# Kernel optimization log

Hardware: AMD Instinct MI355X
Metric: run time of the kernel (lower is better)

Reference implementation:

```python
import jax, jax.numpy as jnp
import numpy as np

SEQ, N = 8192, 1024
W_SYN = 20.0

# ArcTan surrogate spike fn ('ArcTan', alpha=1.0, beta=10.0): forward = Heaviside
@jax.custom_vjp
def spike(x):
    return (x > 0).astype(x.dtype)

def _spike_fwd(x):
    return spike(x), x

def _spike_bwd(x, g):
    return (g * (1.0 / (1.0 + (10.0 * x) ** 2)),)

spike.defvjp(_spike_fwd, _spike_bwd)


def setup_inputs() -> dict:
    key = jax.random.key(0)
    k_in, = jax.random.split(key, 1)
    input_batch = jax.random.normal(k_in, (SEQ, N), dtype=jnp.float32)
    state = jnp.zeros((2, N), jnp.float32)  # (v, u)
    # learned params, sized per init_kwargs
    W1 = jnp.eye(N, dtype=jnp.float32) * W_SYN          # f1.ff.weight [N, N]
    W2 = jnp.ones((1, N), jnp.float32) * W_SYN          # f2.ff.weight [1, N]
    a = jnp.full((N,), 0.02, jnp.float32)
    b = jnp.full((N,), 0.2, jnp.float32)
    c = jnp.full((N,), -65.0, jnp.float32)
    d = jnp.full((N,), 8.0, jnp.float32)
    thresh = jnp.full((N,), 30.0, jnp.float32)
    dt = jnp.full((N,), 1.0, jnp.float32)               # time_step per neuron
    leak = jnp.full((1,), 0.99, jnp.float32)            # decode leak
    return dict(input_batch=input_batch, state=state, W1=W1, W2=W2,
                a=a, b=b, c=c, d=d, thresh=thresh, dt=dt, leak=leak)


def reference(input_batch, state, W1, W2, a, b, c, d, thresh, dt, leak):
    v0, u0 = state[0], state[1]
    dm0 = jnp.zeros((1,), input_batch.dtype)  # decode_mempot starts at 0

    def step(carry, x_t):
        v, u, dm = carry
        I = W1 @ x_t  # synaptic current [N]
        # Izhikevich ODE (Euler step)
        v_new = v + dt * (0.04 * v * v + 5.0 * v + 140.0 - u + I)
        u_new = u + dt * a * (b * v - u)
        s = spike(v_new - thresh)
        v_out = v_new * (1.0 - s) + c * s   # reset v -> c on spike
        u_out = u_new + d * s               # u -> u + d on spike
        dm_new = leak * dm + W2 @ s         # leaky-integrator decode [1]
        return (v_out, u_out, dm_new), (s, jnp.stack([v_out, u_out]), dm_new)

    _, (outputs, states, decoded) = jax.lax.scan(step, (v0, u0, dm0), input_batch)
    return outputs, states, decoded  # [T,N], [T,2,N], [T,1]
```

## Files before the change

kernel.cpp:

```cpp
#include <hip/hip_runtime.h>

#define CAP 32
#define K 32

__global__ void sparsify_kernel(const float* __restrict__ W1, int N,
                                int* __restrict__ cnts, int* __restrict__ cols,
                                float* __restrict__ wts) {
  __shared__ int scnt;
  const int row = blockIdx.x;
  if (threadIdx.x == 0) scnt = 0;
  __syncthreads();
  const float* wr = W1 + (long)row * N;
  for (int k = threadIdx.x; k < N; k += blockDim.x) {
    float w = wr[k];
    if (w != 0.0f) {
      int slot = atomicAdd(&scnt, 1);
      if (slot < CAP) {
        cols[row * CAP + slot] = k;
        wts[row * CAP + slot] = w;
      }
    }
  }
  __syncthreads();
  if (threadIdx.x == 0) {
    cnts[row] = scnt;
    if (scnt == 0) { cols[row * CAP] = 0; wts[row * CAP] = 0.0f; }
  }
}

__global__ void touch_kernel(const float4* __restrict__ x4, long n4,
                             float* __restrict__ dump) {
  long i = (long)blockIdx.x * blockDim.x + threadIdx.x;
  const long stride = (long)gridDim.x * blockDim.x;
  float acc = 0.f;
  for (; i < n4; i += stride) {
    float4 v = x4[i];
    acc += v.x + v.y + v.z + v.w;
  }
  if (acc == 1234.56789f) dump[blockIdx.x & 1023] = acc;
}

#define IZH_STEP(xv, sout)                        \
  {                                               \
    const float I = w0 * (xv);                    \
    float t1 = 0.04f * v;                         \
    float t2 = t1 * v;                            \
    float t3 = 5.0f * v;                          \
    float t4 = t2 + t3;                           \
    float t5 = t4 + 140.0f;                       \
    float t6 = t5 - u;                            \
    float t7 = t6 + I;                            \
    float vn = v + t7;          \
    float q1 = bn * v;                            \
    float q2 = q1 - u;                            \
    float q3 = Pn * q2;                           \
    float un = u + q3;                            \
    float df = vn - thn;                          \
    bool sp = df > 0.0f;                          \
    v = sp ? cn : vn;        \
    u = un + (sp ? dn : 0.0f);   \
    sout = sp ? 1.0f : 0.0f;                      \
  }

__global__ void __launch_bounds__(256) izh_pc_kernel(
    const float* __restrict__ X, const float* __restrict__ state,
    const float* __restrict__ a, const float* __restrict__ b,
    const float* __restrict__ c, const float* __restrict__ d,
    const float* __restrict__ th, const float* __restrict__ dtv,
    const float* __restrict__ W1,
    const int* __restrict__ cnts, const int* __restrict__ cols,
    const float* __restrict__ wts,
    float* __restrict__ o_s, float* __restrict__ o_st,
    int T, int N)
{
#pragma clang fp contract(off)
  __shared__ float obuf[2][K][3][64];
  __shared__ int s_fast;

  const int wid  = threadIdx.x >> 6;
  const int lane = threadIdx.x & 63;
  const int base = blockIdx.x * 64;
  const int gn   = base + lane;
  const long N2  = 2L * N;
  const int B    = T / K;

  if (wid == 0) {
    bool elig = (base + 64 <= N);
    if (elig) elig = (cnts[gn] == 1) && (dtv[gn] == 1.0f);
    unsigned long long m = __ballot(elig);
    if (lane == 0) s_fast = (m == ~0ULL) ? 1 : 0;
  }
  __syncthreads();

  if (s_fast) {
    if (wid == 0) {
      float v = state[gn], u = state[N + gn];
      const float bn = b[gn], cn = c[gn], dn = d[gn], thn = th[gn];
      const float Pn = dtv[gn] * a[gn];
      const float w0 = wts[gn * CAP];
      const int   c0 = cols[gn * CAP];
      const float* Xp = X + c0;

      float xA[K], xB[K];
      if (B >= 1) {
#pragma unroll
        for (int i = 0; i < K; ++i) xA[i] = Xp[(size_t)i * N];
      }

#define COMPUTE(XR, bsel)                                      \
      {                                                        \
        _Pragma("unroll")                                      \
        for (int i = 0; i < K; ++i) {                          \
          float s_;                                            \
          IZH_STEP(XR[i], s_);                                 \
          obuf[bsel][i][0][lane] = s_;                         \
          obuf[bsel][i][1][lane] = v;                          \
          obuf[bsel][i][2][lane] = u;                          \
        }                                                      \
        asm volatile("s_waitcnt lgkmcnt(0)" ::: "memory");     \
        __builtin_amdgcn_s_barrier();                          \
      }

      int k = 0;
      for (; k + 1 < B; k += 2) {
#pragma unroll
        for (int i = 0; i < K; ++i)
          xB[i] = Xp[(size_t)((k + 1) * K + i) * N];
        COMPUTE(xA, 0)
        if (k + 2 < B) {
#pragma unroll
          for (int i = 0; i < K; ++i)
            xA[i] = Xp[(size_t)((k + 2) * K + i) * N];
        }
        COMPUTE(xB, 1)
      }
      if (k < B) COMPUTE(xA, 0)
#undef COMPUTE

      for (int t = B * K; t < T; ++t) {
        float s_;
        IZH_STEP(Xp[(size_t)t * N], s_);
        o_s[(long)t * N + gn] = s_;
        o_st[(long)t * N2 + gn] = v;
        o_st[(long)t * N2 + N + gn] = u;
      }
    } else {
      const int cidx = wid - 1;
      float* P; long RS;
      if (wid == 1)      { P = o_s;      RS = N;  }
      else if (wid == 2) { P = o_st;     RS = N2; }
      else               { P = o_st + N; RS = N2; }
      const int r = lane >> 4, j = lane & 15;

      for (int k = 0; k < B; ++k) {
        if (k > 0) {
          const int q = k - 1, bsel = q & 1, t0 = q * K;
#pragma unroll
          for (int i = 0; i < K; i += 4) {
            float4 val = *(const float4*)&obuf[bsel][i + r][cidx][4 * j];
            *(float4*)(P + (size_t)(t0 + i + r) * RS + base + 4 * j) = val;
          }
        }
        __builtin_amdgcn_s_barrier();
      }
      if (B > 0) {
        const int q = B - 1, bsel = q & 1, t0 = q * K;
#pragma unroll
        for (int i = 0; i < K; i += 4) {
          float4 val = *(const float4*)&obuf[bsel][i + r][cidx][4 * j];
          *(float4*)(P + (size_t)(t0 + i + r) * RS + base + 4 * j) = val;
        }
      }
    }
  } else {
    if (wid != 0 || gn >= N) return;
    float v = state[gn], u = state[N + gn];
    const float an = a[gn], bn = b[gn], cn = c[gn], dn = d[gn];
    const float thn = th[gn], dtn = dtv[gn];
    const float Pn = dtn * an;
    const int cnt = cnts[gn];
    for (int t = 0; t < T; ++t) {
      float I = 0.0f;
      if (cnt <= CAP) {
        for (int j = 0; j < cnt; ++j)
          I = I + wts[gn * CAP + j] * X[(size_t)t * N + cols[gn * CAP + j]];
      } else {
        const float* wr = W1 + (size_t)gn * N;
        const float* xr = X + (size_t)t * N;
        for (int kk = 0; kk < N; ++kk) I = I + wr[kk] * xr[kk];
      }
      float t1 = 0.04f * v; float t2 = t1 * v; float t3 = 5.0f * v;
      float t4 = t2 + t3; float t5 = t4 + 140.0f; float t6 = t5 - u;
      float t7 = t6 + I; float t8 = dtn * t7; float vn = v + t8;
      float q1 = bn * v; float q2 = q1 - u; float q3 = Pn * q2; float un = u + q3;
      float df = vn - thn; bool sp = df > 0.0f;
      v = sp ? cn : vn; u = un + (sp ? dn : 0.0f);
      o_s[(size_t)t * N + gn] = sp ? 1.0f : 0.0f;
      o_st[(size_t)t * N2 + gn] = v;
      o_st[(size_t)t * N2 + N + gn] = u;
    }
  }
}

__global__ void decode_dot_kernel(const float* __restrict__ o_s,
                                  const float* __restrict__ W2,
                                  float* __restrict__ r, int N) {
  const int t = blockIdx.x;
  const float* srow = o_s + (long)t * N;
  float p = 0.0f;
  for (int n = threadIdx.x; n < N; n += blockDim.x)
    p += W2[n] * srow[n];
  for (int off = 32; off > 0; off >>= 1) p += __shfl_down(p, off);
  __shared__ float red[4];
  if ((threadIdx.x & 63) == 0) red[threadIdx.x >> 6] = p;
  __syncthreads();
  if (threadIdx.x == 0) {
    float tot = 0.f;
    const int nw = blockDim.x >> 6;
    for (int w = 0; w < nw; ++w) tot += red[w];
    r[t] = tot;
  }
}

__global__ void decode_scan_kernel(const float* __restrict__ r,
                                   const float* __restrict__ leakp,
                                   float* __restrict__ out, int T) {
  __shared__ float Bsh[64], Ssh[64];
  const float leakv = leakp[0];
  const int i = threadIdx.x;
  const int chunk = (T + 63) / 64;
  const int t0 = i * chunk;
  float B = 0.0f;
  for (int j = 0; j < chunk; ++j) {
    int t = t0 + j;
    if (t < T) B = leakv * B + r[t];
  }
  Bsh[i] = B;
  float A = 1.0f, p = leakv; int e = chunk;
  while (e) { if (e & 1) A *= p; p *= p; e >>= 1; }
  __syncthreads();
  if (i == 0) {
    float dm = 0.0f;
    for (int k = 0; k < 64; ++k) { Ssh[k] = dm; dm = A * dm + Bsh[k]; }
  }
  __syncthreads();
  float dm = Ssh[i];
  for (int j = 0; j < chunk; ++j) {
    int t = t0 + j;
    if (t < T) { dm = leakv * dm + r[t]; out[t] = dm; }
  }
}

extern "C" void kernel_launch(void* const* d_in, const int* in_sizes, int n_in,
                              void* d_out, int out_size, void* d_ws, size_t ws_size,
                              hipStream_t stream) {
  const float* X  = (const float*)d_in[0];
  const float* st = (const float*)d_in[1];
  const float* W1 = (const float*)d_in[2];
  const float* W2 = (const float*)d_in[3];
  const float* a  = (const float*)d_in[4];
  const float* b  = (const float*)d_in[5];
  const float* c  = (const float*)d_in[6];
  const float* d  = (const float*)d_in[7];
  const float* th = (const float*)d_in[8];
  const float* dt = (const float*)d_in[9];
  const float* lk = (const float*)d_in[10];
  const int N = in_sizes[4];
  const int T = in_sizes[0] / N;

  float* o_s  = (float*)d_out;
  float* o_st = o_s + (long)T * N;
  float* o_dm = o_st + 2L * (long)T * N;

  int*   cnts = (int*)d_ws;
  int*   cols = cnts + N;
  float* wts  = (float*)(cols + (long)N * CAP);
  float* rbuf = wts + (long)N * CAP;
  float* dump = rbuf + T;

  sparsify_kernel<<<N, 256, 0, stream>>>(W1, N, cnts, cols, wts);
  const long n4 = ((long)T * N) / 4;
  touch_kernel<<<1024, 256, 0, stream>>>((const float4*)X, n4, dump);
  const int nblk = (N + 63) / 64;
  izh_pc_kernel<<<nblk, 256, 0, stream>>>(X, st, a, b, c, d, th, dt, W1,
                                          cnts, cols, wts, o_s, o_st, T, N);
  decode_dot_kernel<<<T, 256, 0, stream>>>(o_s, W2, rbuf, N);
  decode_scan_kernel<<<1, 64, 0, stream>>>(rbuf, lk, o_dm, T);
}
```

Before: 616.3 us.

## Pack two neuron groups per block, halve chunk size, raise compute-wave priority

Each block now holds two independent 64-neuron sets, each with its own compute wave and three store waves, so launches use 512 threads over half as many blocks. The time-chunk size K drops from 32 to 16, which shrinks per-wave register arrays and the shared buffers, and the compute wave gets raised scheduling priority during the recurrence. The aim is a shorter serial critical path per compute wave, with stores overlapping more finely. In exchange, the two sets share barriers, so each waits on the slower one, and there are only 8 blocks for N=1024, so fewer CUs are occupied.

New measurement: 771.3 us. 1.25x slower.

```diff
diff --git a/kernel.cpp b/kernel.cpp
--- a/kernel.cpp
+++ b/kernel.cpp
@@ -1,7 +1,7 @@
 #include <hip/hip_runtime.h>
 
 #define CAP 32
-#define K 32
+#define K 16
 
 __global__ void sparsify_kernel(const float* __restrict__ W1, int N,
                                 int* __restrict__ cnts, int* __restrict__ cols,
@@ -62,7 +62,7 @@
     sout = sp ? 1.0f : 0.0f;                      \
   }
 
-__global__ void __launch_bounds__(256) izh_pc_kernel(
+__global__ void __launch_bounds__(512) izh_pc2_kernel(
     const float* __restrict__ X, const float* __restrict__ state,
     const float* __restrict__ a, const float* __restrict__ b,
     const float* __restrict__ c, const float* __restrict__ d,
@@ -74,26 +74,30 @@
     int T, int N)
 {
 #pragma clang fp contract(off)
-  __shared__ float obuf[2][K][3][64];
-  __shared__ int s_fast;
+  __shared__ float obuf[2][2][K][3][64];
+  __shared__ int s_ok[2];
 
   const int wid  = threadIdx.x >> 6;
   const int lane = threadIdx.x & 63;
-  const int base = blockIdx.x * 64;
+  const int role = wid & 3;
+  const int set  = wid >> 2;
+  const int base = blockIdx.x * 128 + set * 64;
   const int gn   = base + lane;
   const long N2  = 2L * N;
   const int B    = T / K;
 
-  if (wid == 0) {
+  if (role == 0) {
     bool elig = (base + 64 <= N);
     if (elig) elig = (cnts[gn] == 1) && (dtv[gn] == 1.0f);
     unsigned long long m = __ballot(elig);
-    if (lane == 0) s_fast = (m == ~0ULL) ? 1 : 0;
-  }
-  __syncthreads();
-
-  if (s_fast) {
-    if (wid == 0) {
+    if (lane == 0) s_ok[set] = (m == ~0ULL) ? 1 : 0;
+  }
+  __syncthreads();
+  const bool fast = (s_ok[0] != 0) && (s_ok[1] != 0);
+
+  if (fast) {
+    if (role == 0) {
+      __builtin_amdgcn_s_setprio(1);
       float v = state[gn], u = state[N + gn];
       const float bn = b[gn], cn = c[gn], dn = d[gn], thn = th[gn];
       const float Pn = dtv[gn] * a[gn];
@@ -113,9 +117,9 @@
         for (int i = 0; i < K; ++i) {                          \
           float s_;                                            \
           IZH_STEP(XR[i], s_);                                 \
-          obuf[bsel][i][0][lane] = s_;                         \
-          obuf[bsel][i][1][lane] = v;                          \
-          obuf[bsel][i][2][lane] = u;                          \
+          obuf[set][bsel][i][0][lane] = s_;                    \
+          obuf[set][bsel][i][1][lane] = v;                     \
+          obuf[set][bsel][i][2][lane] = u;                     \
         }                                                      \
         asm volatile("s_waitcnt lgkmcnt(0)" ::: "memory");     \
         __builtin_amdgcn_s_barrier();                          \
@@ -136,6 +140,7 @@
       }
       if (k < B) COMPUTE(xA, 0)
 #undef COMPUTE
+      __builtin_amdgcn_s_setprio(0);
 
       for (int t = B * K; t < T; ++t) {
         float s_;
@@ -145,11 +150,11 @@
         o_st[(long)t * N2 + N + gn] = u;
       }
     } else {
-      const int cidx = wid - 1;
+      const int cidx = role - 1;
       float* P; long RS;
-      if (wid == 1)      { P = o_s;      RS = N;  }
-      else if (wid == 2) { P = o_st;     RS = N2; }
-      else               { P = o_st + N; RS = N2; }
+      if (role == 1)      { P = o_s;      RS = N;  }
+      else if (role == 2) { P = o_st;     RS = N2; }
+      else                { P = o_st + N; RS = N2; }
       const int r = lane >> 4, j = lane & 15;
 
       for (int k = 0; k < B; ++k) {
@@ -157,7 +162,7 @@
           const int q = k - 1, bsel = q & 1, t0 = q * K;
 #pragma unroll
           for (int i = 0; i < K; i += 4) {
-            float4 val = *(const float4*)&obuf[bsel][i + r][cidx][4 * j];
+            float4 val = *(const float4*)&obuf[set][bsel][i + r][cidx][4 * j];
             *(float4*)(P + (size_t)(t0 + i + r) * RS + base + 4 * j) = val;
           }
         }
@@ -167,13 +172,13 @@
         const int q = B - 1, bsel = q & 1, t0 = q * K;
 #pragma unroll
         for (int i = 0; i < K; i += 4) {
-          float4 val = *(const float4*)&obuf[bsel][i + r][cidx][4 * j];
+          float4 val = *(const float4*)&obuf[set][bsel][i + r][cidx][4 * j];
           *(float4*)(P + (size_t)(t0 + i + r) * RS + base + 4 * j) = val;
         }
       }
     }
   } else {
-    if (wid != 0 || gn >= N) return;
+    if (role != 0 || gn >= N) return;
     float v = state[gn], u = state[N + gn];
     const float an = a[gn], bn = b[gn], cn = c[gn], dn = d[gn];
     const float thn = th[gn], dtn = dtv[gn];
@@ -281,9 +286,9 @@
   sparsify_kernel<<<N, 256, 0, stream>>>(W1, N, cnts, cols, wts);
   const long n4 = ((long)T * N) / 4;
   touch_kernel<<<1024, 256, 0, stream>>>((const float4*)X, n4, dump);
-  const int nblk = (N + 63) / 64;
-  izh_pc_kernel<<<nblk, 256, 0, stream>>>(X, st, a, b, c, d, th, dt, W1,
-                                          cnts, cols, wts, o_s, o_st, T, N);
+  const int nblk = (N + 127) / 128;
+  izh_pc2_kernel<<<nblk, 512, 0, stream>>>(X, st, a, b, c, d, th, dt, W1,
+                                           cnts, cols, wts, o_s, o_st, T, N);
   decode_dot_kernel<<<T, 256, 0, stream>>>(o_s, W2, rbuf, N);
   decode_scan_kernel<<<1, 64, 0, stream>>>(rbuf, lk, o_dm, T);
 }
```

## Offload input loading and spike/reset selection from the serial Izhikevich wave

Applied to the files above, without the earlier changes.

The single compute wave used to load X from global memory, multiply by the weight, and perform the spike test and reset before buffering s, v and u. Now a producer wave prefetches the weighted input into a double-buffered LDS buffer one block ahead. The compute wave only integrates the ODE and stores the pre-reset vn and un. The three writer waves each recompute the spike test or the reset from vn/un and the thresholds before streaming their output to global memory. This shortens the per-step critical path of the serial recurrence, at the cost of an extra LDS read per step and duplicated threshold comparisons in the writer waves.

Result: faster. 513.2 us (-16.7%).

```diff
diff --git a/kernel.cpp b/kernel.cpp
--- a/kernel.cpp
+++ b/kernel.cpp
@@ -40,29 +40,7 @@
   if (acc == 1234.56789f) dump[blockIdx.x & 1023] = acc;
 }
 
-#define IZH_STEP(xv, sout)                        \
-  {                                               \
-    const float I = w0 * (xv);                    \
-    float t1 = 0.04f * v;                         \
-    float t2 = t1 * v;                            \
-    float t3 = 5.0f * v;                          \
-    float t4 = t2 + t3;                           \
-    float t5 = t4 + 140.0f;                       \
-    float t6 = t5 - u;                            \
-    float t7 = t6 + I;                            \
-    float vn = v + t7;          \
-    float q1 = bn * v;                            \
-    float q2 = q1 - u;                            \
-    float q3 = Pn * q2;                           \
-    float un = u + q3;                            \
-    float df = vn - thn;                          \
-    bool sp = df > 0.0f;                          \
-    v = sp ? cn : vn;        \
-    u = un + (sp ? dn : 0.0f);   \
-    sout = sp ? 1.0f : 0.0f;                      \
-  }
-
-__global__ void __launch_bounds__(256) izh_pc_kernel(
+__global__ void __launch_bounds__(256) izh_pc3_kernel(
     const float* __restrict__ X, const float* __restrict__ state,
     const float* __restrict__ a, const float* __restrict__ b,
     const float* __restrict__ c, const float* __restrict__ d,
@@ -74,7 +52,8 @@
     int T, int N)
 {
 #pragma clang fp contract(off)
-  __shared__ float obuf[2][K][3][64];
+  __shared__ float ibuf[2][K][64];
+  __shared__ float obuf[2][K][2][64];
   __shared__ int s_fast;
 
   const int wid  = threadIdx.x >> 6;
@@ -93,72 +72,128 @@
   __syncthreads();
 
   if (s_fast) {
+    if (wid == 1) {
+      const float wn = wts[gn * CAP];
+      const int   c0 = cols[gn * CAP];
+      const float* Xp = X + c0;
+      float xr[K];
+#pragma unroll
+      for (int i = 0; i < K; ++i) xr[i] = Xp[(size_t)i * N];
+#pragma unroll
+      for (int i = 0; i < K; ++i) ibuf[0][i][lane] = wn * xr[i];
+    }
+    __syncthreads();
+
     if (wid == 0) {
       float v = state[gn], u = state[N + gn];
       const float bn = b[gn], cn = c[gn], dn = d[gn], thn = th[gn];
       const float Pn = dtv[gn] * a[gn];
-      const float w0 = wts[gn * CAP];
+
+      for (int k = 0; k < B; ++k) {
+        const int bsel = k & 1;
+#pragma unroll
+        for (int i = 0; i < K; ++i) {
+          const float I = ibuf[bsel][i][lane];
+          float t1 = 0.04f * v;
+          float t2 = t1 * v;
+          float t3 = 5.0f * v;
+          float t4 = t2 + t3;
+          float t5 = t4 + 140.0f;
+          float t6 = t5 - u;
+          float t7 = t6 + I;
+          float vn = v + t7;
+          float q1 = bn * v;
+          float q2 = q1 - u;
+          float q3 = Pn * q2;
+          float un = u + q3;
+          obuf[bsel][i][0][lane] = vn;
+          obuf[bsel][i][1][lane] = un;
+          bool sp = vn > thn;
+          v = sp ? cn : vn;
+          u = un + (sp ? dn : 0.0f);
+        }
+        asm volatile("s_waitcnt lgkmcnt(0)" ::: "memory");
+        __builtin_amdgcn_s_barrier();
+      }
+
+      if (B * K < T) {
+        const float w0 = wts[gn * CAP];
+        const float* Xp = X + cols[gn * CAP];
+        for (int t = B * K; t < T; ++t) {
+          const float I = w0 * Xp[(size_t)t * N];
+          float t1 = 0.04f * v; float t2 = t1 * v; float t3 = 5.0f * v;
+          float t4 = t2 + t3; float t5 = t4 + 140.0f; float t6 = t5 - u;
+          float t7 = t6 + I; float vn = v + t7;
+          float q1 = bn * v; float q2 = q1 - u; float q3 = Pn * q2;
+          float un = u + q3;
+          bool sp = vn > thn;
+          v = sp ? cn : vn; u = un + (sp ? dn : 0.0f);
+          o_s[(long)t * N + gn] = sp ? 1.0f : 0.0f;
+          o_st[(long)t * N2 + gn] = v;
+          o_st[(long)t * N2 + N + gn] = u;
+        }
+      }
+    } else if (wid == 1) {
+      const float wn = wts[gn * CAP];
       const int   c0 = cols[gn * CAP];
       const float* Xp = X + c0;
-
-      float xA[K], xB[K];
-      if (B >= 1) {
-#pragma unroll
-        for (int i = 0; i < K; ++i) xA[i] = Xp[(size_t)i * N];
-      }
-
-#define COMPUTE(XR, bsel)                                      \
-      {                                                        \
-        _Pragma("unroll")                                      \
-        for (int i = 0; i < K; ++i) {                          \
-          float s_;                                            \
-          IZH_STEP(XR[i], s_);                                 \
-          obuf[bsel][i][0][lane] = s_;                         \
-          obuf[bsel][i][1][lane] = v;                          \
-          obuf[bsel][i][2][lane] = u;                          \
-        }                                                      \
-        asm volatile("s_waitcnt lgkmcnt(0)" ::: "memory");     \
-        __builtin_amdgcn_s_barrier();                          \
-      }
-
-      int k = 0;
-      for (; k + 1 < B; k += 2) {
-#pragma unroll
-        for (int i = 0; i < K; ++i)
-          xB[i] = Xp[(size_t)((k + 1) * K + i) * N];
-        COMPUTE(xA, 0)
-        if (k + 2 < B) {
-#pragma unroll
-          for (int i = 0; i < K; ++i)
-            xA[i] = Xp[(size_t)((k + 2) * K + i) * N];
-        }
-        COMPUTE(xB, 1)
-      }
-      if (k < B) COMPUTE(xA, 0)
-#undef COMPUTE
-
-      for (int t = B * K; t < T; ++t) {
-        float s_;
-        IZH_STEP(Xp[(size_t)t * N], s_);
-        o_s[(long)t * N + gn] = s_;
-        o_st[(long)t * N2 + gn] = v;
-        o_st[(long)t * N2 + N + gn] = u;
-      }
-    } else {
-      const int cidx = wid - 1;
-      float* P; long RS;
-      if (wid == 1)      { P = o_s;      RS = N;  }
-      else if (wid == 2) { P = o_st;     RS = N2; }
-      else               { P = o_st + N; RS = N2; }
       const int r = lane >> 4, j = lane & 15;
+      const float4 th4 = *(const float4*)&th[base + 4 * j];
+
+      for (int k = 0; k < B; ++k) {
+        if (k + 1 < B) {
+          float xr[K];
+#pragma unroll
+          for (int i = 0; i < K; ++i) xr[i] = Xp[(size_t)((k + 1) * K + i) * N];
+#pragma unroll
+          for (int i = 0; i < K; ++i) ibuf[(k + 1) & 1][i][lane] = wn * xr[i];
+        }
+        if (k > 0) {
+          const int q = k - 1, bsel = q & 1, t0 = q * K;
+#pragma unroll
+          for (int i = 0; i < K; i += 4) {
+            float4 vn4 = *(const float4*)&obuf[bsel][i + r][0][4 * j];
+            float4 s4;
+            s4.x = vn4.x > th4.x ? 1.0f : 0.0f;
+            s4.y = vn4.y > th4.y ? 1.0f : 0.0f;
+            s4.z = vn4.z > th4.z ? 1.0f : 0.0f;
+            s4.w = vn4.w > th4.w ? 1.0f : 0.0f;
+            *(float4*)(o_s + (size_t)(t0 + i + r) * N + base + 4 * j) = s4;
+          }
+        }
+        asm volatile("s_waitcnt lgkmcnt(0)" ::: "memory");
+        __builtin_amdgcn_s_barrier();
+      }
+      if (B > 0) {
+        const int q = B - 1, bsel = q & 1, t0 = q * K;
+#pragma unroll
+        for (int i = 0; i < K; i += 4) {
+          float4 vn4 = *(const float4*)&obuf[bsel][i + r][0][4 * j];
+          float4 s4;
+          s4.x = vn4.x > th4.x ? 1.0f : 0.0f;
+          s4.y = vn4.y > th4.y ? 1.0f : 0.0f;
+          s4.z = vn4.z > th4.z ? 1.0f : 0.0f;
+          s4.w = vn4.w > th4.w ? 1.0f : 0.0f;
+          *(float4*)(o_s + (size_t)(t0 + i + r) * N + base + 4 * j) = s4;
+        }
+      }
+    } else if (wid == 2) {
+      const int r = lane >> 4, j = lane & 15;
+      const float4 th4 = *(const float4*)&th[base + 4 * j];
+      const float4 c4  = *(const float4*)&c[base + 4 * j];
 
       for (int k = 0; k < B; ++k) {
         if (k > 0) {
           const int q = k - 1, bsel = q & 1, t0 = q * K;
 #pragma unroll
           for (int i = 0; i < K; i += 4) {
-            float4 val = *(const float4*)&obuf[bsel][i + r][cidx][4 * j];
-            *(float4*)(P + (size_t)(t0 + i + r) * RS + base + 4 * j) = val;
+            float4 vn4 = *(const float4*)&obuf[bsel][i + r][0][4 * j];
+            float4 o4;
+            o4.x = vn4.x > th4.x ? c4.x : vn4.x;
+            o4.y = vn4.y > th4.y ? c4.y : vn4.y;
+            o4.z = vn4.z > th4.z ? c4.z : vn4.z;
+            o4.w = vn4.w > th4.w ? c4.w : vn4.w;
+            *(float4*)(o_st + (size_t)(t0 + i + r) * N2 + base + 4 * j) = o4;
           }
         }
         __builtin_amdgcn_s_barrier();
@@ -167,8 +202,49 @@
         const int q = B - 1, bsel = q & 1, t0 = q * K;
 #pragma unroll
         for (int i = 0; i < K; i += 4) {
-          float4 val = *(const float4*)&obuf[bsel][i + r][cidx][4 * j];
-          *(float4*)(P + (size_t)(t0 + i + r) * RS + base + 4 * j) = val;
+          float4 vn4 = *(const float4*)&obuf[bsel][i + r][0][4 * j];
+          float4 o4;
+          o4.x = vn4.x > th4.x ? c4.x : vn4.x;
+          o4.y = vn4.y > th4.y ? c4.y : vn4.y;
+          o4.z = vn4.z > th4.z ? c4.z : vn4.z;
+          o4.w = vn4.w > th4.w ? c4.w : vn4.w;
+          *(float4*)(o_st + (size_t)(t0 + i + r) * N2 + base + 4 * j) = o4;
+        }
+      }
+    } else {
+      const int r = lane >> 4, j = lane & 15;
+      const float4 th4 = *(const float4*)&th[base + 4 * j];
+      const float4 d4  = *(const float4*)&d[base + 4 * j];
+
+      for (int k = 0; k < B; ++k) {
+        if (k > 0) {
+          const int q = k - 1, bsel = q & 1, t0 = q * K;
+#pragma unroll
+          for (int i = 0; i < K; i += 4) {
+            float4 vn4 = *(const float4*)&obuf[bsel][i + r][0][4 * j];
+            float4 un4 = *(const float4*)&obuf[bsel][i + r][1][4 * j];
+            float4 o4;
+            o4.x = un4.x + (vn4.x > th4.x ? d4.x : 0.0f);
+            o4.y = un4.y + (vn4.y > th4.y ? d4.y : 0.0f);
+            o4.z = un4.z + (vn4.z > th4.z ? d4.z : 0.0f);
+            o4.w = un4.w + (vn4.w > th4.w ? d4.w : 0.0f);
+            *(float4*)(o_st + (size_t)(t0 + i + r) * N2 + N + base + 4 * j) = o4;
+          }
+        }
+        __builtin_amdgcn_s_barrier();
+      }
+      if (B > 0) {
+        const int q = B - 1, bsel = q & 1, t0 = q * K;
+#pragma unroll
+        for (int i = 0; i < K; i += 4) {
+          float4 vn4 = *(const float4*)&obuf[bsel][i + r][0][4 * j];
+          float4 un4 = *(const float4*)&obuf[bsel][i + r][1][4 * j];
+          float4 o4;
+          o4.x = un4.x + (vn4.x > th4.x ? d4.x : 0.0f);
+          o4.y = un4.y + (vn4.y > th4.y ? d4.y : 0.0f);
+          o4.z = un4.z + (vn4.z > th4.z ? d4.z : 0.0f);
+          o4.w = un4.w + (vn4.w > th4.w ? d4.w : 0.0f);
+          *(float4*)(o_st + (size_t)(t0 + i + r) * N2 + N + base + 4 * j) = o4;
         }
       }
     }
@@ -282,8 +358,8 @@
   const long n4 = ((long)T * N) / 4;
   touch_kernel<<<1024, 256, 0, stream>>>((const float4*)X, n4, dump);
   const int nblk = (N + 63) / 64;
-  izh_pc_kernel<<<nblk, 256, 0, stream>>>(X, st, a, b, c, d, th, dt, W1,
-                                          cnts, cols, wts, o_s, o_st, T, N);
+  izh_pc3_kernel<<<nblk, 256, 0, stream>>>(X, st, a, b, c, d, th, dt, W1,
+                                           cnts, cols, wts, o_s, o_st, T, N);
   decode_dot_kernel<<<T, 256, 0, stream>>>(o_s, W2, rbuf, N);
   decode_scan_kernel<<<1, 64, 0, stream>>>(rbuf, lk, o_dm, T);
 }
```
